# Kernel tuning notes

Measured on AMD Instinct MI355X. Metric: run time of the kernel, lower is better.

The kernel has to match this reference:

```python
import jax, jax.numpy as jnp
import numpy as np

NUM_EMBEDDINGS = 1024
EMBEDDING_DIM = 64
COMMITMENT_COST = 0.25


def setup_inputs() -> dict:
    key = jax.random.key(0)
    kz, kc = jax.random.split(key)
    z = jax.random.normal(kz, (16, 2048, EMBEDDING_DIM), dtype=jnp.float32)
    # nn.Embedding weight init: uniform(-1/K, 1/K)
    codebook = (jax.random.uniform(kc, (NUM_EMBEDDINGS, EMBEDDING_DIM), dtype=jnp.float32) * 2.0 - 1.0) / NUM_EMBEDDINGS
    return {"z": z, "codebook": codebook}


def reference(z, codebook):
    D = codebook.shape[1]
    K = codebook.shape[0]
    flat_z = z.reshape(-1, D)  # [N, D]
    # squared L2 distances: ||z||^2 + ||e||^2 - 2 z.e  -> [N, K]
    distances = (
        jnp.sum(flat_z ** 2, axis=1, keepdims=True)
        + jnp.sum(codebook ** 2, axis=1)
        - 2.0 * jnp.matmul(flat_z, codebook.T)
    )
    encoding_indices = jnp.argmin(distances, axis=1)  # [N]
    quantized = codebook[encoding_indices].reshape(z.shape)

    e_latent_loss = jnp.mean((jax.lax.stop_gradient(quantized) - z) ** 2)
    q_latent_loss = jnp.mean((quantized - jax.lax.stop_gradient(z)) ** 2)
    vq_loss = q_latent_loss + COMMITMENT_COST * e_latent_loss

    # straight-through estimator
    quantized_st = z + jax.lax.stop_gradient(quantized - z)

    # perplexity from codebook usage histogram
    n = encoding_indices.shape[0]
    counts = jnp.zeros((K,), dtype=jnp.float32).at[encoding_indices].add(1.0)
    avg_probs = counts / n
    perplexity = jnp.exp(-jnp.sum(avg_probs * jnp.log(avg_probs + 1e-10)))

    indices_out = encoding_indices.reshape(z.shape[:-1])
    return quantized_st, vq_loss, indices_out, perplexity
```

## Files before the change

### kernel.cpp

```cpp
#include <hip/hip_runtime.h>
#include <math.h>


#define D 64
#define KC 1024
#define MT 4
#define ROWS (MT * 16)

typedef short short8 __attribute__((ext_vector_type(8)));
typedef short short4v __attribute__((ext_vector_type(4)));
typedef float f32x4 __attribute__((ext_vector_type(4)));

__device__ __forceinline__ unsigned short f2bf(float x) {
  unsigned int u = __float_as_uint(x);
  unsigned int r = (u + 0x7fffu + ((u >> 16) & 1u)) >> 16;
  return (unsigned short)r;
}
__device__ __forceinline__ float bf2f(unsigned short h) {
  return __uint_as_float((unsigned int)h << 16);
}

__global__ __launch_bounds__(256) void vq_prep(
    const float* __restrict__ cb, const float* __restrict__ z,
    unsigned short* __restrict__ bsplit, unsigned short* __restrict__ zsplit,
    float* __restrict__ cbn, float* __restrict__ rzn,
    unsigned int* __restrict__ hist, float* __restrict__ loss_acc) {
  __shared__ float srzp[1024];
  const int b = blockIdx.x;
  const int tid = threadIdx.x;
  if (b < 4) {
    const int k = b * 256 + tid;
    const float4* e = (const float4*)(cb + (size_t)k * D);
    unsigned short* bp = bsplit + (size_t)k * 128;
    float s0 = 0.f, s1 = 0.f, s2 = 0.f, s3 = 0.f;
#pragma unroll
    for (int i = 0; i < 16; ++i) {
      float4 v = e[i];
      s0 = fmaf(v.x, v.x, s0);
      s1 = fmaf(v.y, v.y, s1);
      s2 = fmaf(v.z, v.z, s2);
      s3 = fmaf(v.w, v.w, s3);
      unsigned short h0 = f2bf(v.x), h1 = f2bf(v.y), h2 = f2bf(v.z),
                     h3 = f2bf(v.w);
      short4v hv = {(short)h0, (short)h1, (short)h2, (short)h3};
      short4v lv = {(short)f2bf(v.x - bf2f(h0)), (short)f2bf(v.y - bf2f(h1)),
                    (short)f2bf(v.z - bf2f(h2)), (short)f2bf(v.w - bf2f(h3))};
      *(short4v*)(bp + i * 4) = hv;
      *(short4v*)(bp + 64 + i * 4) = lv;
    }
    cbn[k] = (s0 + s1) + (s2 + s3);
    hist[k] = 0u;
    if (k == 0) loss_acc[0] = 0.f;
  } else {
    const int rowbase = (b - 4) * 64;
    const float4* z4 = (const float4*)(z + (size_t)rowbase * D);
#pragma unroll
    for (int it = 0; it < 4; ++it) {
      int f4 = it * 256 + tid;
      int row = f4 >> 4, c4 = (f4 & 15) * 4;
      float4 v = z4[f4];
      srzp[f4] = ((v.x * v.x + v.y * v.y) + (v.z * v.z + v.w * v.w));
      unsigned short h0 = f2bf(v.x), h1 = f2bf(v.y), h2 = f2bf(v.z),
                     h3 = f2bf(v.w);
      short4v hv = {(short)h0, (short)h1, (short)h2, (short)h3};
      short4v lv = {(short)f2bf(v.x - bf2f(h0)), (short)f2bf(v.y - bf2f(h1)),
                    (short)f2bf(v.z - bf2f(h2)), (short)f2bf(v.w - bf2f(h3))};
      unsigned short* zp = zsplit + (size_t)(rowbase + row) * 128;
      *(short4v*)(zp + c4) = hv;
      *(short4v*)(zp + 64 + c4) = lv;
    }
    __syncthreads();
    if (tid < 64) {
      float s = 0.f;
#pragma unroll
      for (int i = 0; i < 16; ++i) s += srzp[tid * 16 + i];
      rzn[rowbase + tid] = s;
    }
  }
}

__global__ __launch_bounds__(256, 2) void vq_score(
    const unsigned short* __restrict__ zsplit, const float* __restrict__ rzn,
    const unsigned short* __restrict__ bsplit, const float* __restrict__ cbn,
    float* __restrict__ t2d, int* __restrict__ t2k) {
  __shared__ float candd[4][ROWS][17];
  __shared__ int candk[4][ROWS][17];

  const int tid = threadIdx.x;
  const int lane = tid & 63;
  const int wav = tid >> 6;
  const int quad = lane >> 4;
  const int col = lane & 15;
  const int rowbase = blockIdx.x * ROWS;

  short8 a[MT][4];
#pragma unroll
  for (int mt = 0; mt < MT; ++mt) {
    const unsigned short* base =
        zsplit + (size_t)(rowbase + mt * 16 + col) * 128 + quad * 8;
    a[mt][0] = *(const short8*)(base + 0);
    a[mt][1] = *(const short8*)(base + 32);
    a[mt][2] = *(const short8*)(base + 64);
    a[mt][3] = *(const short8*)(base + 96);
  }
  float rzv[MT * 4];
#pragma unroll
  for (int mt = 0; mt < MT; ++mt)
#pragma unroll
    for (int reg = 0; reg < 4; ++reg)
      rzv[mt * 4 + reg] = rzn[rowbase + mt * 16 + quad * 4 + reg];

  float bestd[MT * 4];
  int bestk[MT * 4];
#pragma unroll
  for (int i = 0; i < MT * 4; ++i) {
    bestd[i] = 3.4e38f;
    bestk[i] = 0;
  }

  const int k0 = wav * 256;
  short8 p0[4], p1[4];
  float pe0, pe1;
  {
    const unsigned short* b0p = bsplit + (size_t)(k0 + col) * 128 + quad * 8;
    p0[0] = *(const short8*)(b0p + 0);
    p0[1] = *(const short8*)(b0p + 32);
    p0[2] = *(const short8*)(b0p + 64);
    p0[3] = *(const short8*)(b0p + 96);
    pe0 = cbn[k0 + col];
    const unsigned short* b1p =
        bsplit + (size_t)(k0 + 16 + col) * 128 + quad * 8;
    p1[0] = *(const short8*)(b1p + 0);
    p1[1] = *(const short8*)(b1p + 32);
    p1[2] = *(const short8*)(b1p + 64);
    p1[3] = *(const short8*)(b1p + 96);
    pe1 = cbn[k0 + 16 + col];
  }

  for (int it = 0; it < 8; ++it) {
    const short8 c00 = p0[0], c01 = p0[1], c02 = p0[2], c03 = p0[3];
    const short8 c10 = p1[0], c11 = p1[1], c12 = p1[2], c13 = p1[3];
    const float ce0 = pe0, ce1 = pe1;
    const int kbase = k0 + it * 32;
    if (it < 7) {
      const unsigned short* n0 =
          bsplit + (size_t)(kbase + 32 + col) * 128 + quad * 8;
      p0[0] = *(const short8*)(n0 + 0);
      p0[1] = *(const short8*)(n0 + 32);
      p0[2] = *(const short8*)(n0 + 64);
      p0[3] = *(const short8*)(n0 + 96);
      pe0 = cbn[kbase + 32 + col];
      const unsigned short* n1 =
          bsplit + (size_t)(kbase + 48 + col) * 128 + quad * 8;
      p1[0] = *(const short8*)(n1 + 0);
      p1[1] = *(const short8*)(n1 + 32);
      p1[2] = *(const short8*)(n1 + 64);
      p1[3] = *(const short8*)(n1 + 96);
      pe1 = cbn[kbase + 48 + col];
    }
    {
      f32x4 acc[MT];
#pragma unroll
      for (int mt = 0; mt < MT; ++mt) acc[mt] = {0.f, 0.f, 0.f, 0.f};
#pragma unroll
      for (int mt = 0; mt < MT; ++mt)
        acc[mt] = __builtin_amdgcn_mfma_f32_16x16x32_bf16(a[mt][0], c00, acc[mt], 0, 0, 0);
#pragma unroll
      for (int mt = 0; mt < MT; ++mt)
        acc[mt] = __builtin_amdgcn_mfma_f32_16x16x32_bf16(a[mt][1], c01, acc[mt], 0, 0, 0);
#pragma unroll
      for (int mt = 0; mt < MT; ++mt)
        acc[mt] = __builtin_amdgcn_mfma_f32_16x16x32_bf16(a[mt][2], c00, acc[mt], 0, 0, 0);
#pragma unroll
      for (int mt = 0; mt < MT; ++mt)
        acc[mt] = __builtin_amdgcn_mfma_f32_16x16x32_bf16(a[mt][3], c01, acc[mt], 0, 0, 0);
#pragma unroll
      for (int mt = 0; mt < MT; ++mt)
        acc[mt] = __builtin_amdgcn_mfma_f32_16x16x32_bf16(a[mt][0], c02, acc[mt], 0, 0, 0);
#pragma unroll
      for (int mt = 0; mt < MT; ++mt)
        acc[mt] = __builtin_amdgcn_mfma_f32_16x16x32_bf16(a[mt][1], c03, acc[mt], 0, 0, 0);
      const int mycode = kbase + col;
#pragma unroll
      for (int mt = 0; mt < MT; ++mt)
#pragma unroll
        for (int reg = 0; reg < 4; ++reg) {
          float dist = fmaf(-2.0f, acc[mt][reg], rzv[mt * 4 + reg] + ce0);
          int i = mt * 4 + reg;
          bool better = dist < bestd[i];
          bestk[i] = better ? mycode : bestk[i];
          bestd[i] = better ? dist : bestd[i];
        }
    }
    {
      f32x4 acc[MT];
#pragma unroll
      for (int mt = 0; mt < MT; ++mt) acc[mt] = {0.f, 0.f, 0.f, 0.f};
#pragma unroll
      for (int mt = 0; mt < MT; ++mt)
        acc[mt] = __builtin_amdgcn_mfma_f32_16x16x32_bf16(a[mt][0], c10, acc[mt], 0, 0, 0);
#pragma unroll
      for (int mt = 0; mt < MT; ++mt)
        acc[mt] = __builtin_amdgcn_mfma_f32_16x16x32_bf16(a[mt][1], c11, acc[mt], 0, 0, 0);
#pragma unroll
      for (int mt = 0; mt < MT; ++mt)
        acc[mt] = __builtin_amdgcn_mfma_f32_16x16x32_bf16(a[mt][2], c10, acc[mt], 0, 0, 0);
#pragma unroll
      for (int mt = 0; mt < MT; ++mt)
        acc[mt] = __builtin_amdgcn_mfma_f32_16x16x32_bf16(a[mt][3], c11, acc[mt], 0, 0, 0);
#pragma unroll
      for (int mt = 0; mt < MT; ++mt)
        acc[mt] = __builtin_amdgcn_mfma_f32_16x16x32_bf16(a[mt][0], c12, acc[mt], 0, 0, 0);
#pragma unroll
      for (int mt = 0; mt < MT; ++mt)
        acc[mt] = __builtin_amdgcn_mfma_f32_16x16x32_bf16(a[mt][1], c13, acc[mt], 0, 0, 0);
      const int mycode = kbase + 16 + col;
#pragma unroll
      for (int mt = 0; mt < MT; ++mt)
#pragma unroll
        for (int reg = 0; reg < 4; ++reg) {
          float dist = fmaf(-2.0f, acc[mt][reg], rzv[mt * 4 + reg] + ce1);
          int i = mt * 4 + reg;
          bool better = dist < bestd[i];
          bestk[i] = better ? mycode : bestk[i];
          bestd[i] = better ? dist : bestd[i];
        }
    }
  }

#pragma unroll
  for (int mt = 0; mt < MT; ++mt)
#pragma unroll
    for (int reg = 0; reg < 4; ++reg) {
      int row = mt * 16 + quad * 4 + reg;
      candd[wav][row][col] = bestd[mt * 4 + reg];
      candk[wav][row][col] = bestk[mt * 4 + reg];
    }
  __syncthreads();

  if (tid < ROWS) {
    float bd1 = 3.4e38f, bd2 = 3.4e38f;
    int bk1 = 0x7fffffff, bk2 = 0x7fffffff;
#pragma unroll
    for (int w = 0; w < 4; ++w)
      for (int c = 0; c < 16; ++c) {
        float dv = candd[w][tid][c];
        int kv = candk[w][tid][c];
        bool h1 = (dv < bd1) || (dv == bd1 && kv < bk1);
        bool h2 = (dv < bd2) || (dv == bd2 && kv < bk2);
        if (h1) {
          bd2 = bd1; bk2 = bk1;
          bd1 = dv; bk1 = kv;
        } else if (h2) {
          bd2 = dv; bk2 = kv;
        }
      }
    const int row = rowbase + tid;
    t2d[2 * row] = bd1;
    t2d[2 * row + 1] = bd2;
    t2k[2 * row] = bk1;
    t2k[2 * row + 1] = bk2;
  }
}

__global__ __launch_bounds__(256) void vq_writer(
    const float* __restrict__ z, const float* __restrict__ cb,
    const float* __restrict__ cbn, const float* __restrict__ t2d,
    const int* __restrict__ t2k, float* __restrict__ out_q,
    float* __restrict__ out_idx, unsigned int* __restrict__ hist,
    float* __restrict__ loss_acc) {
  __shared__ int skf[ROWS];
  __shared__ unsigned int lhist[KC];
  __shared__ float swav[4];
  const int tid = threadIdx.x;
  const int lane = tid & 63;
  const int wav = tid >> 6;
  const int rowbase = blockIdx.x * ROWS;

#pragma unroll
  for (int j = 0; j < KC / 256; ++j) lhist[tid + 256 * j] = 0u;
  __syncthreads();

  if (tid < ROWS) {
    const int row = rowbase + tid;
    float bd1 = t2d[2 * row], bd2 = t2d[2 * row + 1];
    int bk1 = t2k[2 * row], bk2 = t2k[2 * row + 1];
    if (bd2 - bd1 < 1e-5f) {
      const float4* zp = (const float4*)(z + (size_t)row * D);
      float s0 = 0.f, s1 = 0.f, s2 = 0.f, s3 = 0.f;
#pragma unroll
      for (int i = 0; i < 16; ++i) {
        float4 v = zp[i];
        s0 = fmaf(v.x, v.x, s0);
        s1 = fmaf(v.y, v.y, s1);
        s2 = fmaf(v.z, v.z, s2);
        s3 = fmaf(v.w, v.w, s3);
      }
      const float rzx = (s0 + s1) + (s2 + s3);
      float dx[2];
      int kk[2] = {bk1, bk2};
#pragma unroll
      for (int c = 0; c < 2; ++c) {
        const float4* e4 = (const float4*)(cb + (size_t)kk[c] * D);
        float d0 = 0.f, d1 = 0.f, d2 = 0.f, d3 = 0.f;
#pragma unroll
        for (int i = 0; i < 16; ++i) {
          float4 v = e4[i];
          float4 zv = zp[i];
          d0 = fmaf(zv.x, v.x, d0);
          d1 = fmaf(zv.y, v.y, d1);
          d2 = fmaf(zv.z, v.z, d2);
          d3 = fmaf(zv.w, v.w, d3);
        }
        float dot = (d0 + d1) + (d2 + d3);
        dx[c] = (rzx + cbn[kk[c]]) - 2.0f * dot;
      }
      if ((dx[1] < dx[0]) || (dx[1] == dx[0] && bk2 < bk1)) bk1 = bk2;
    }
    skf[tid] = bk1;
    out_idx[row] = (float)bk1;
    atomicAdd(&lhist[bk1], 1u);
  }
  __syncthreads();

#pragma unroll
  for (int j = 0; j < KC / 256; ++j) {
    unsigned int c = lhist[tid + 256 * j];
    if (c) atomicAdd(&hist[tid + 256 * j], c);
  }

  float lsum = 0.f;
#pragma unroll
  for (int it = 0; it < 4; ++it) {
    int f4 = it * 256 + tid;
    int r = f4 >> 4;
    int c4 = (f4 & 15) * 4;
    int bk = skf[r];
    const float4 q = *(const float4*)(cb + (size_t)bk * D + c4);
    const int grow = rowbase + r;
    const float4 zv = *(const float4*)(z + (size_t)grow * D + c4);
    *(float4*)(out_q + (size_t)grow * D + c4) = q;
    float ax = q.x - zv.x, ay = q.y - zv.y, az = q.z - zv.z, aw = q.w - zv.w;
    lsum += ax * ax + ay * ay + az * az + aw * aw;
  }
#pragma unroll
  for (int off = 32; off > 0; off >>= 1) lsum += __shfl_down(lsum, off, 64);
  if (lane == 0) swav[wav] = lsum;
  __syncthreads();
  if (tid == 0)
    atomicAdd(loss_acc, (swav[0] + swav[1]) + (swav[2] + swav[3]));
}

__global__ __launch_bounds__(1024) void vq_final(
    const unsigned int* __restrict__ hist, const float* __restrict__ loss_acc,
    float* __restrict__ out_loss, float* __restrict__ out_perp, float inv_n,
    float inv_nd) {
  __shared__ float part[16];
  const int t = threadIdx.x;
  const int lane = t & 63;
  const int wav = t >> 6;
  float p = (float)hist[t] * inv_n;
  float v = p * logf(p + 1e-10f);
#pragma unroll
  for (int off = 32; off > 0; off >>= 1) v += __shfl_down(v, off, 64);
  if (lane == 0) part[wav] = v;
  __syncthreads();
  if (t == 0) {
    float s = 0.f;
#pragma unroll
    for (int j = 0; j < 16; ++j) s += part[j];
    *out_perp = expf(-s);
    *out_loss = 1.25f * loss_acc[0] * inv_nd;
  }
}

extern "C" void kernel_launch(void* const* d_in, const int* in_sizes, int n_in,
                              void* d_out, int out_size, void* d_ws,
                              size_t ws_size, hipStream_t stream) {
  (void)n_in;
  (void)out_size;
  (void)ws_size;
  const float* z = (const float*)d_in[0];
  const float* cb = (const float*)d_in[1];
  const int N = in_sizes[0] / D;

  float* out_q = (float*)d_out;
  float* out_loss = (float*)d_out + (size_t)N * D;
  float* out_idx = out_loss + 1;
  float* out_perp = out_idx + N;

  unsigned int* hist = (unsigned int*)d_ws;
  float* loss_acc = (float*)d_ws + 1024;
  float* cbn = (float*)d_ws + 1040;
  unsigned short* bsplit = (unsigned short*)((float*)d_ws + 2064);
  unsigned short* zsplit = (unsigned short*)((float*)d_ws + 67600);
  float* rzn = (float*)d_ws + 2164752;
  float* t2d = (float*)d_ws + 2197520;
  int* t2k = (int*)((float*)d_ws + 2263056);

  vq_prep<<<dim3(4 + N / 64), dim3(256), 0, stream>>>(cb, z, bsplit, zsplit,
                                                      cbn, rzn, hist, loss_acc);
  vq_score<<<dim3(N / ROWS), dim3(256), 0, stream>>>(zsplit, rzn, bsplit, cbn,
                                                     t2d, t2k);
  vq_writer<<<dim3(N / ROWS), dim3(256), 0, stream>>>(
      z, cb, cbn, t2d, t2k, out_q, out_idx, hist, loss_acc);
  vq_final<<<dim3(1), dim3(1024), 0, stream>>>(
      hist, loss_acc, out_loss, out_perp, 1.0f / (float)N,
      1.0f / ((float)N * (float)D));
}
```

Baseline: 114.6 us.

## Split codebook search across two blocks per row tile and merge top-2 in writer

The score kernel now launches twice as many blocks. Each block scans half of the codebook (512 entries, 128 per wave) for its 64-row tile instead of all 1024. Each half writes its own top-2 candidates to a wider scratch buffer, and the writer kernel merges the four candidates per row. This is meant to raise parallelism and occupancy across the GPU's compute units. The cost is reloading the z fragments twice, an extra per-block reduction, and more scratch traffic.

```diff
diff --git a/kernel.cpp b/kernel.cpp
--- a/kernel.cpp
+++ b/kernel.cpp
@@ -91,7 +91,8 @@
   const int wav = tid >> 6;
   const int quad = lane >> 4;
   const int col = lane & 15;
-  const int rowbase = blockIdx.x * ROWS;
+  const int half = blockIdx.x & 1;
+  const int rowbase = (blockIdx.x >> 1) * ROWS;
 
   short8 a[MT][4];
 #pragma unroll
@@ -118,7 +119,7 @@
     bestk[i] = 0;
   }
 
-  const int k0 = wav * 256;
+  const int k0 = half * 512 + wav * 128;
   short8 p0[4], p1[4];
   float pe0, pe1;
   {
@@ -137,12 +138,12 @@
     pe1 = cbn[k0 + 16 + col];
   }
 
-  for (int it = 0; it < 8; ++it) {
+  for (int it = 0; it < 4; ++it) {
     const short8 c00 = p0[0], c01 = p0[1], c02 = p0[2], c03 = p0[3];
     const short8 c10 = p1[0], c11 = p1[1], c12 = p1[2], c13 = p1[3];
     const float ce0 = pe0, ce1 = pe1;
     const int kbase = k0 + it * 32;
-    if (it < 7) {
+    if (it < 3) {
       const unsigned short* n0 =
           bsplit + (size_t)(kbase + 32 + col) * 128 + quad * 8;
       p0[0] = *(const short8*)(n0 + 0);
@@ -256,10 +257,10 @@
         }
       }
     const int row = rowbase + tid;
-    t2d[2 * row] = bd1;
-    t2d[2 * row + 1] = bd2;
-    t2k[2 * row] = bk1;
-    t2k[2 * row + 1] = bk2;
+    t2d[row * 4 + half * 2] = bd1;
+    t2d[row * 4 + half * 2 + 1] = bd2;
+    t2k[row * 4 + half * 2] = bk1;
+    t2k[row * 4 + half * 2 + 1] = bk2;
   }
 }
 
@@ -283,8 +284,23 @@
 
   if (tid < ROWS) {
     const int row = rowbase + tid;
-    float bd1 = t2d[2 * row], bd2 = t2d[2 * row + 1];
-    int bk1 = t2k[2 * row], bk2 = t2k[2 * row + 1];
+    const float4 dv = *(const float4*)&t2d[row * 4];
+    const int4 kv = *(const int4*)&t2k[row * 4];
+    float cd[4] = {dv.x, dv.y, dv.z, dv.w};
+    int ck[4] = {kv.x, kv.y, kv.z, kv.w};
+    float bd1 = 3.4e38f, bd2 = 3.4e38f;
+    int bk1 = 0x7fffffff, bk2 = 0x7fffffff;
+#pragma unroll
+    for (int c = 0; c < 4; ++c) {
+      bool h1 = (cd[c] < bd1) || (cd[c] == bd1 && ck[c] < bk1);
+      bool h2 = (cd[c] < bd2) || (cd[c] == bd2 && ck[c] < bk2);
+      if (h1) {
+        bd2 = bd1; bk2 = bk1;
+        bd1 = cd[c]; bk1 = ck[c];
+      } else if (h2) {
+        bd2 = cd[c]; bk2 = ck[c];
+      }
+    }
     if (bd2 - bd1 < 1e-5f) {
       const float4* zp = (const float4*)(z + (size_t)row * D);
       float s0 = 0.f, s1 = 0.f, s2 = 0.f, s3 = 0.f;
@@ -396,12 +412,12 @@
   unsigned short* zsplit = (unsigned short*)((float*)d_ws + 67600);
   float* rzn = (float*)d_ws + 2164752;
   float* t2d = (float*)d_ws + 2197520;
-  int* t2k = (int*)((float*)d_ws + 2263056);
+  int* t2k = (int*)((float*)d_ws + 2328592);
 
   vq_prep<<<dim3(4 + N / 64), dim3(256), 0, stream>>>(cb, z, bsplit, zsplit,
                                                       cbn, rzn, hist, loss_acc);
-  vq_score<<<dim3(N / ROWS), dim3(256), 0, stream>>>(zsplit, rzn, bsplit, cbn,
-                                                     t2d, t2k);
+  vq_score<<<dim3(2 * (N / ROWS)), dim3(256), 0, stream>>>(zsplit, rzn, bsplit,
+                                                           cbn, t2d, t2k);
   vq_writer<<<dim3(N / ROWS), dim3(256), 0, stream>>>(
       z, cb, cbn, t2d, t2k, out_q, out_idx, hist, loss_acc);
   vq_final<<<dim3(1), dim3(1024), 0, stream>>>(
```

New measurement: 124.4 us. +8.6%, slower.
